# Performance work log

Measured on AMD Instinct MI355X. Metric: run time of the kernel, lower is better.

Reference implementation:

```python
import jax, jax.numpy as jnp
import numpy as np

WIN = 7  # skimage structural_similarity default win_size


def _uniform_valid(x):
    # x: [N, H, W] -> [N, H-6, W-6]; 7x7 uniform (box) filter, VALID.
    # exactly equivalent to uniform_filter + crop (boundary mode irrelevant).
    k = jnp.ones((1, 1, WIN, WIN), x.dtype) / (WIN * WIN)
    y = jax.lax.conv_general_dilated(x[:, None], k, (1, 1), 'VALID')
    return y[:, 0]


def _ssim_frames(x, y):
    # K1=0.01, K2=0.03, data_range=255, sample covariance (N/(N-1)).
    C1 = (0.01 * 255.0) ** 2
    C2 = (0.03 * 255.0) ** 2
    NP = WIN * WIN
    cov_norm = NP / (NP - 1.0)
    ux = _uniform_valid(x)
    uy = _uniform_valid(y)
    uxx = _uniform_valid(x * x)
    uyy = _uniform_valid(y * y)
    uxy = _uniform_valid(x * y)
    vx = cov_norm * (uxx - ux * ux)
    vy = cov_norm * (uyy - uy * uy)
    vxy = cov_norm * (uxy - ux * uy)
    S = ((2.0 * ux * uy + C1) * (2.0 * vxy + C2)) / (
        (ux * ux + uy * uy + C1) * (vx + vy + C2))
    return jnp.mean(S, axis=(1, 2))  # per-frame mean SSIM


def setup_inputs() -> dict:
    key = jax.random.key(0)
    k1, k2, k3 = jax.random.split(key, 3)
    B, T, C, H, W = 8, 20, 1, 512, 512
    gen_img = jax.random.uniform(k1, (B, T, C, H, W), dtype=jnp.float32)
    target = jax.random.uniform(k2, (B, T, C, H, W), dtype=jnp.float32)
    gen_D = jax.random.normal(k3, (B, 1), dtype=jnp.float32)
    return {"gen_img": gen_img, "target": target, "gen_D": gen_D}


def reference(gen_img, target, gen_D):
    B, T, C, H, W = gen_img.shape
    diff = gen_img - target
    L_rec = jnp.mean(jnp.abs(diff)) + jnp.mean(diff * diff)
    # SSIM on channel 0 of every frame, scaled by 255 (as in the numpy loop);
    # original detaches, so stop_gradient for faithfulness.
    x = gen_img[:, :, 0].reshape(B * T, H, W) * 255.0
    y = target[:, :, 0].reshape(B * T, H, W) * 255.0
    L_ssim = jnp.mean(jax.lax.stop_gradient(_ssim_frames(x, y)))
    L_adv = -jnp.mean(gen_D)
    L_total = L_rec + 0.01 * (1.0 - L_ssim) + 0.0001 * L_adv
    return (L_total, L_rec, L_ssim, L_adv)
```

## Files before the change

### kernel.cpp

```cpp
#include <hip/hip_runtime.h>

#define FRAMES 160
#define HH 512
#define WW 512
#define STRIPS 8
#define SROWS 64
#define NTOT 41943040
#define NBLK (STRIPS * FRAMES)


__device__ __forceinline__ float ssim_val(float Sx, float Sy, float Sxx,
                                          float Syy, float Sxy) {
  const float inv_np = 1.0f / 49.0f;
  const float cov = 49.0f / 48.0f;
  const float C1 = 1.0e-4f;
  const float C2 = 9.0e-4f;
  float ux = Sx * inv_np, uy = Sy * inv_np;
  float vx = cov * (Sxx * inv_np - ux * ux);
  float vy = cov * (Syy * inv_np - uy * uy);
  float vxy = cov * (Sxy * inv_np - ux * uy);
  float A1 = 2.0f * ux * uy + C1;
  float A2 = 2.0f * vxy + C2;
  float B1 = ux * ux + uy * uy + C1;
  float B2 = vx + vy + C2;
  return (A1 * A2) / (B1 * B2);
}

__global__ __launch_bounds__(256) void fused_kernel(
    const float* __restrict__ g, const float* __restrict__ t,
    float* __restrict__ ws) {
  const int strip = blockIdx.x;
  const int frame = blockIdx.y;
  const int row0 = strip * SROWS;
  const int rows = (strip == STRIPS - 1) ? 58 : 64;
  const int tid = threadIdx.x;
  const float* __restrict__ gf = g + (size_t)frame * (HH * WW) + tid * 2;
  const float* __restrict__ tf = t + (size_t)frame * (HH * WW) + tid * 2;

  __shared__ float2 buf[2][5][256];

  float2 xr[6], yr[6];
  float2 Sx = {0.f, 0.f}, Sy = {0.f, 0.f};
  float2 Sxx = {0.f, 0.f}, Syy = {0.f, 0.f}, Sxy = {0.f, 0.f};
  float sabs = 0.f, ssq = 0.f, ssum = 0.f;

  #pragma unroll
  for (int i = 0; i < 6; ++i) {
    float2 xv = *(const float2*)(gf + (row0 + i) * WW);
    float2 yv = *(const float2*)(tf + (row0 + i) * WW);
    xr[i] = xv; yr[i] = yv;
    float dx = xv.x - yv.x, dy = xv.y - yv.y;
    sabs += fabsf(dx) + fabsf(dy);
    ssq += dx * dx + dy * dy;
    Sx.x += xv.x; Sx.y += xv.y;
    Sy.x += yv.x; Sy.y += yv.y;
    Sxx.x += xv.x * xv.x; Sxx.y += xv.y * xv.y;
    Syy.x += yv.x * yv.x; Syy.y += yv.y * yv.y;
    Sxy.x += xv.x * yv.x; Sxy.y += xv.y * yv.y;
  }

  for (int r = 0; r < rows; ++r) {
    float2 nx = *(const float2*)(gf + (row0 + r + 6) * WW);
    float2 ny = *(const float2*)(tf + (row0 + r + 6) * WW);
    if (r < 58) {
      float dx = nx.x - ny.x, dy = nx.y - ny.y;
      sabs += fabsf(dx) + fabsf(dy);
      ssq += dx * dx + dy * dy;
    }
    Sx.x += nx.x; Sx.y += nx.y;
    Sy.x += ny.x; Sy.y += ny.y;
    Sxx.x += nx.x * nx.x; Sxx.y += nx.y * nx.y;
    Syy.x += ny.x * ny.x; Syy.y += ny.y * ny.y;
    Sxy.x += nx.x * ny.x; Sxy.y += nx.y * ny.y;

    const int par = r & 1;
    float px = Sx.x + Sx.y, py = Sy.x + Sy.y;
    float pxx = Sxx.x + Sxx.y, pyy = Syy.x + Syy.y, pxy = Sxy.x + Sxy.y;
    buf[par][0][tid] = make_float2(Sx.x, px);
    buf[par][1][tid] = make_float2(Sy.x, py);
    buf[par][2][tid] = make_float2(Sxx.x, pxx);
    buf[par][3][tid] = make_float2(Syy.x, pyy);
    buf[par][4][tid] = make_float2(Sxy.x, pxy);
    __syncthreads();

    if (tid < 253) {
      const float2* bx = buf[par][0];
      const float2* by = buf[par][1];
      const float2* bxx = buf[par][2];
      const float2* byy = buf[par][3];
      const float2* bxy = buf[par][4];
      float p1, p2; float2 f3;
      p1 = bx[tid + 1].y; p2 = bx[tid + 2].y; f3 = bx[tid + 3];
      float wxe = px + p1 + p2 + f3.x;
      float wxo = Sx.y + p1 + p2 + f3.y;
      p1 = by[tid + 1].y; p2 = by[tid + 2].y; f3 = by[tid + 3];
      float wye = py + p1 + p2 + f3.x;
      float wyo = Sy.y + p1 + p2 + f3.y;
      p1 = bxx[tid + 1].y; p2 = bxx[tid + 2].y; f3 = bxx[tid + 3];
      float wxxe = pxx + p1 + p2 + f3.x;
      float wxxo = Sxx.y + p1 + p2 + f3.y;
      p1 = byy[tid + 1].y; p2 = byy[tid + 2].y; f3 = byy[tid + 3];
      float wyye = pyy + p1 + p2 + f3.x;
      float wyyo = Syy.y + p1 + p2 + f3.y;
      p1 = bxy[tid + 1].y; p2 = bxy[tid + 2].y; f3 = bxy[tid + 3];
      float wxye = pxy + p1 + p2 + f3.x;
      float wxyo = Sxy.y + p1 + p2 + f3.y;

      ssum += ssim_val(wxe, wye, wxxe, wyye, wxye);
      ssum += ssim_val(wxo, wyo, wxxo, wyyo, wxyo);
    }

    float2 ox = xr[0], oy = yr[0];
    Sx.x -= ox.x; Sx.y -= ox.y;
    Sy.x -= oy.x; Sy.y -= oy.y;
    Sxx.x -= ox.x * ox.x; Sxx.y -= ox.y * ox.y;
    Syy.x -= oy.x * oy.x; Syy.y -= oy.y * oy.y;
    Sxy.x -= ox.x * oy.x; Sxy.y -= ox.y * oy.y;
    #pragma unroll
    for (int i = 0; i < 5; ++i) { xr[i] = xr[i + 1]; yr[i] = yr[i + 1]; }
    xr[5] = nx; yr[5] = ny;
  }

  #pragma unroll
  for (int off = 32; off > 0; off >>= 1) {
    sabs += __shfl_down(sabs, off, 64);
    ssq += __shfl_down(ssq, off, 64);
    ssum += __shfl_down(ssum, off, 64);
  }
  __syncthreads();
  float* scr = (float*)buf;
  const int lane = tid & 63, wv = tid >> 6;
  if (lane == 0) { scr[wv] = sabs; scr[4 + wv] = ssq; scr[8 + wv] = ssum; }
  __syncthreads();
  if (tid == 0) {
    const int bid = blockIdx.y * STRIPS + blockIdx.x;
    ws[bid] = scr[0] + scr[1] + scr[2] + scr[3];
    ws[NBLK + bid] = scr[4] + scr[5] + scr[6] + scr[7];
    ws[2 * NBLK + bid] = scr[8] + scr[9] + scr[10] + scr[11];
  }
}

__global__ __launch_bounds__(256) void finalize_kernel(
    const float* __restrict__ ws, const float* __restrict__ genD,
    float* __restrict__ out) {
  const int tid = threadIdx.x;
  float a = 0.f, b = 0.f, c = 0.f;
  for (int i = tid; i < NBLK; i += 256) {
    a += ws[i];
    b += ws[NBLK + i];
    c += ws[2 * NBLK + i];
  }
  #pragma unroll
  for (int off = 32; off > 0; off >>= 1) {
    a += __shfl_down(a, off, 64);
    b += __shfl_down(b, off, 64);
    c += __shfl_down(c, off, 64);
  }
  __shared__ float la[4], lb[4], lc[4];
  const int lane = tid & 63, wv = tid >> 6;
  if (lane == 0) { la[wv] = a; lb[wv] = b; lc[wv] = c; }
  __syncthreads();
  if (tid == 0) {
    a = la[0] + la[1] + la[2] + la[3];
    b = lb[0] + lb[1] + lb[2] + lb[3];
    c = lc[0] + lc[1] + lc[2] + lc[3];
    const float invN = 1.0f / (float)NTOT;
    float L_rec = a * invN + b * invN;
    float L_ssim = c / (160.0f * 506.0f * 506.0f);
    float d = 0.f;
    #pragma unroll
    for (int i = 0; i < 8; ++i) d += genD[i];
    float L_adv = -d / 8.0f;
    float L_total = L_rec + 0.01f * (1.0f - L_ssim) + 0.0001f * L_adv;
    out[0] = L_total;
    out[1] = L_rec;
    out[2] = L_ssim;
    out[3] = L_adv;
  }
}

extern "C" void kernel_launch(void* const* d_in, const int* in_sizes, int n_in,
                              void* d_out, int out_size, void* d_ws,
                              size_t ws_size, hipStream_t stream) {
  const float* gen_img = (const float*)d_in[0];
  const float* target = (const float*)d_in[1];
  const float* gen_D = (const float*)d_in[2];
  float* out = (float*)d_out;
  float* ws = (float*)d_ws;

  dim3 grid(STRIPS, FRAMES);
  fused_kernel<<<grid, 256, 0, stream>>>(gen_img, target, ws);
  finalize_kernel<<<1, 256, 0, stream>>>(ws, gen_D, out);
}
```

Before: 367.6 us.

## Restructure SSIM sliding window to float4 columns with two row groups per block

Result: slower. 375.9 us (+2.2%).

```diff
diff --git a/kernel.cpp b/kernel.cpp
--- a/kernel.cpp
+++ b/kernel.cpp
@@ -3,122 +3,124 @@
 #define FRAMES 160
 #define HH 512
 #define WW 512
-#define STRIPS 8
-#define SROWS 64
+#define STRIPS 16
+#define NBLK (STRIPS * FRAMES)
 #define NTOT 41943040
-#define NBLK (STRIPS * FRAMES)
 
-
-__device__ __forceinline__ float ssim_val(float Sx, float Sy, float Sxx,
-                                          float Syy, float Sxy) {
-  const float inv_np = 1.0f / 49.0f;
-  const float cov = 49.0f / 48.0f;
-  const float C1 = 1.0e-4f;
-  const float C2 = 9.0e-4f;
-  float ux = Sx * inv_np, uy = Sy * inv_np;
-  float vx = cov * (Sxx * inv_np - ux * ux);
-  float vy = cov * (Syy * inv_np - uy * uy);
-  float vxy = cov * (Sxy * inv_np - ux * uy);
-  float A1 = 2.0f * ux * uy + C1;
-  float A2 = 2.0f * vxy + C2;
-  float B1 = ux * ux + uy * uy + C1;
-  float B2 = vx + vy + C2;
-  return (A1 * A2) / (B1 * B2);
+__device__ __forceinline__ float ssim_fast(float a, float b, float sxx,
+                                           float syy, float sxy) {
+  const float K1 = 0.2401f;
+  const float K2 = 2.1609f;
+  const float cA = 49.0f / 24.0f;
+  const float cB = 49.0f / 48.0f;
+  float ab = a * b;
+  float s2 = fmaf(a, a, b * b);
+  float A1 = fmaf(2.0f, ab, K1);
+  float B1 = s2 + K1;
+  float A2 = fmaf(cA, fmaf(49.0f, sxy, -ab), K2);
+  float B2 = fmaf(cB, fmaf(49.0f, sxx + syy, -s2), K2);
+  return (A1 * A2) * __builtin_amdgcn_rcpf(B1 * B2);
 }
 
+#define HSTORE(S, P, A)                          \
+  P.x = S.x; P.y = P.x + S.y;                    \
+  P.z = P.y + S.z; P.w = P.z + S.w;              \
+  lds[grp][A][0][q] = make_float2(P.x, P.y);     \
+  lds[grp][A][1][q] = make_float2(P.z, P.w);
+
+#define HWIN(P, W, A) {                          \
+  float2 h1 = lds[grp][A][1][q + 1];             \
+  float2 l2 = lds[grp][A][0][q + 2];             \
+  W.x = P.w + h1.x;                              \
+  W.y = (P.w - P.x) + h1.y;                      \
+  W.z = (P.w - P.y) + (h1.y + l2.x);             \
+  W.w = (P.w - P.z) + (h1.y + l2.y); }
+
+#define LREC(xv, yv) {                                         \
+  float4 d_ = make_float4(xv.x - yv.x, xv.y - yv.y,            \
+                          xv.z - yv.z, xv.w - yv.w);           \
+  sabs += fabsf(d_.x) + fabsf(d_.y) + fabsf(d_.z) + fabsf(d_.w); \
+  ssq += d_.x * d_.x + d_.y * d_.y;                            \
+  ssq += d_.z * d_.z + d_.w * d_.w; }
+
+#define VADD(xv, yv)                                    \
+  Sx += xv; Sy += yv;                                   \
+  Sxx += xv * xv; Syy += yv * yv; Sxy += xv * yv;
+
+#define VSUB(xv, yv)                                    \
+  Sx -= xv; Sy -= yv;                                   \
+  Sxx -= xv * xv; Syy -= yv * yv; Sxy -= xv * yv;
+
 __global__ __launch_bounds__(256) void fused_kernel(
-    const float* __restrict__ g, const float* __restrict__ t,
+    const float* __restrict__ gsrc, const float* __restrict__ tsrc,
     float* __restrict__ ws) {
   const int strip = blockIdx.x;
   const int frame = blockIdx.y;
-  const int row0 = strip * SROWS;
-  const int rows = (strip == STRIPS - 1) ? 58 : 64;
+  const int row0 = strip * 32;
+  const int n_iter = (strip == STRIPS - 1) ? 13 : 16;
   const int tid = threadIdx.x;
-  const float* __restrict__ gf = g + (size_t)frame * (HH * WW) + tid * 2;
-  const float* __restrict__ tf = t + (size_t)frame * (HH * WW) + tid * 2;
+  const int grp = tid >> 7;
+  const int q = tid & 127;
 
-  __shared__ float2 buf[2][5][256];
+  const float* gp = gsrc + ((size_t)frame * HH + row0 + grp) * WW + q * 4;
+  const float* tp = tsrc + ((size_t)frame * HH + row0 + grp) * WW + q * 4;
 
-  float2 xr[6], yr[6];
-  float2 Sx = {0.f, 0.f}, Sy = {0.f, 0.f};
-  float2 Sxx = {0.f, 0.f}, Syy = {0.f, 0.f}, Sxy = {0.f, 0.f};
+  __shared__ float2 lds[2][5][2][132];
+
+  float4 Sx = make_float4(0.f, 0.f, 0.f, 0.f);
+  float4 Sy = Sx, Sxx = Sx, Syy = Sx, Sxy = Sx;
   float sabs = 0.f, ssq = 0.f, ssum = 0.f;
 
-  #pragma unroll
-  for (int i = 0; i < 6; ++i) {
-    float2 xv = *(const float2*)(gf + (row0 + i) * WW);
-    float2 yv = *(const float2*)(tf + (row0 + i) * WW);
-    xr[i] = xv; yr[i] = yv;
-    float dx = xv.x - yv.x, dy = xv.y - yv.y;
-    sabs += fabsf(dx) + fabsf(dy);
-    ssq += dx * dx + dy * dy;
-    Sx.x += xv.x; Sx.y += xv.y;
-    Sy.x += yv.x; Sy.y += yv.y;
-    Sxx.x += xv.x * xv.x; Sxx.y += xv.y * xv.y;
-    Syy.x += yv.x * yv.x; Syy.y += yv.y * yv.y;
-    Sxy.x += xv.x * yv.x; Sxy.y += xv.y * yv.y;
+  for (int i = 0; i < 7; ++i) {
+    float4 xv = *(const float4*)(gp + i * WW);
+    float4 yv = *(const float4*)(tp + i * WW);
+    VADD(xv, yv)
+    if (grp == 0) { LREC(xv, yv) }
   }
 
-  for (int r = 0; r < rows; ++r) {
-    float2 nx = *(const float2*)(gf + (row0 + r + 6) * WW);
-    float2 ny = *(const float2*)(tf + (row0 + r + 6) * WW);
-    if (r < 58) {
-      float dx = nx.x - ny.x, dy = nx.y - ny.y;
-      sabs += fabsf(dx) + fabsf(dy);
-      ssq += dx * dx + dy * dy;
-    }
-    Sx.x += nx.x; Sx.y += nx.y;
-    Sy.x += ny.x; Sy.y += ny.y;
-    Sxx.x += nx.x * nx.x; Sxx.y += nx.y * nx.y;
-    Syy.x += ny.x * ny.x; Syy.y += ny.y * ny.y;
-    Sxy.x += nx.x * ny.x; Sxy.y += nx.y * ny.y;
-
-    const int par = r & 1;
-    float px = Sx.x + Sx.y, py = Sy.x + Sy.y;
-    float pxx = Sxx.x + Sxx.y, pyy = Syy.x + Syy.y, pxy = Sxy.x + Sxy.y;
-    buf[par][0][tid] = make_float2(Sx.x, px);
-    buf[par][1][tid] = make_float2(Sy.x, py);
-    buf[par][2][tid] = make_float2(Sxx.x, pxx);
-    buf[par][3][tid] = make_float2(Syy.x, pyy);
-    buf[par][4][tid] = make_float2(Sxy.x, pxy);
+  for (int it = 0; it < n_iter; ++it) {
+    float4 Px, Py, Pxx, Pyy, Pxy;
+    HSTORE(Sx, Px, 0) HSTORE(Sy, Py, 1) HSTORE(Sxx, Pxx, 2)
+    HSTORE(Syy, Pyy, 3) HSTORE(Sxy, Pxy, 4)
+    __syncthreads();
+    float4 Wx, Wy, Wxx, Wyy, Wxy;
+    HWIN(Px, Wx, 0) HWIN(Py, Wy, 1) HWIN(Pxx, Wxx, 2)
+    HWIN(Pyy, Wyy, 3) HWIN(Pxy, Wxy, 4)
+    float v0 = ssim_fast(Wx.x, Wy.x, Wxx.x, Wyy.x, Wxy.x);
+    float v1 = ssim_fast(Wx.y, Wy.y, Wxx.y, Wyy.y, Wxy.y);
+    float v2 = ssim_fast(Wx.z, Wy.z, Wxx.z, Wyy.z, Wxy.z);
+    float v3 = ssim_fast(Wx.w, Wy.w, Wxx.w, Wyy.w, Wxy.w);
+    ssum += (q <= 126) ? v0 : 0.f;
+    ssum += (q <= 126) ? v1 : 0.f;
+    ssum += (q <= 125) ? v2 : 0.f;
+    ssum += (q <= 125) ? v3 : 0.f;
     __syncthreads();
 
-    if (tid < 253) {
-      const float2* bx = buf[par][0];
-      const float2* by = buf[par][1];
-      const float2* bxx = buf[par][2];
-      const float2* byy = buf[par][3];
-      const float2* bxy = buf[par][4];
-      float p1, p2; float2 f3;
-      p1 = bx[tid + 1].y; p2 = bx[tid + 2].y; f3 = bx[tid + 3];
-      float wxe = px + p1 + p2 + f3.x;
-      float wxo = Sx.y + p1 + p2 + f3.y;
-      p1 = by[tid + 1].y; p2 = by[tid + 2].y; f3 = by[tid + 3];
-      float wye = py + p1 + p2 + f3.x;
-      float wyo = Sy.y + p1 + p2 + f3.y;
-      p1 = bxx[tid + 1].y; p2 = bxx[tid + 2].y; f3 = bxx[tid + 3];
-      float wxxe = pxx + p1 + p2 + f3.x;
-      float wxxo = Sxx.y + p1 + p2 + f3.y;
-      p1 = byy[tid + 1].y; p2 = byy[tid + 2].y; f3 = byy[tid + 3];
-      float wyye = pyy + p1 + p2 + f3.x;
-      float wyyo = Syy.y + p1 + p2 + f3.y;
-      p1 = bxy[tid + 1].y; p2 = bxy[tid + 2].y; f3 = bxy[tid + 3];
-      float wxye = pxy + p1 + p2 + f3.x;
-      float wxyo = Sxy.y + p1 + p2 + f3.y;
-
-      ssum += ssim_val(wxe, wye, wxxe, wyye, wxye);
-      ssum += ssim_val(wxo, wyo, wxxo, wyyo, wxyo);
+    if (it + 1 < n_iter) {
+      const float* pn = gp + (size_t)(2 * it + 7) * WW;
+      const float* qn = tp + (size_t)(2 * it + 7) * WW;
+      const float* po = gp + (size_t)(2 * it) * WW;
+      const float* qo = tp + (size_t)(2 * it) * WW;
+      {
+        float4 nx = *(const float4*)pn;
+        float4 ny = *(const float4*)qn;
+        float4 ox = *(const float4*)po;
+        float4 oy = *(const float4*)qo;
+        VADD(nx, ny)
+        VSUB(ox, oy)
+        if ((grp == 0) && (2 * it + 7 <= 30)) { LREC(nx, ny) }
+      }
+      {
+        float4 nx = *(const float4*)(pn + WW);
+        float4 ny = *(const float4*)(qn + WW);
+        float4 ox = *(const float4*)(po + WW);
+        float4 oy = *(const float4*)(qo + WW);
+        VADD(nx, ny)
+        VSUB(ox, oy)
+        bool cnt = (grp == 0) ? (2 * it + 8 <= 30) : (2 * it + 9 == 31);
+        if (cnt) { LREC(nx, ny) }
+      }
     }
-
-    float2 ox = xr[0], oy = yr[0];
-    Sx.x -= ox.x; Sx.y -= ox.y;
-    Sy.x -= oy.x; Sy.y -= oy.y;
-    Sxx.x -= ox.x * ox.x; Sxx.y -= ox.y * ox.y;
-    Syy.x -= oy.x * oy.x; Syy.y -= oy.y * oy.y;
-    Sxy.x -= ox.x * oy.x; Sxy.y -= ox.y * oy.y;
-    #pragma unroll
-    for (int i = 0; i < 5; ++i) { xr[i] = xr[i + 1]; yr[i] = yr[i + 1]; }
-    xr[5] = nx; yr[5] = ny;
   }
 
   #pragma unroll
@@ -127,8 +129,7 @@
     ssq += __shfl_down(ssq, off, 64);
     ssum += __shfl_down(ssum, off, 64);
   }
-  __syncthreads();
-  float* scr = (float*)buf;
+  float* scr = (float*)&lds[0][0][0][0];
   const int lane = tid & 63, wv = tid >> 6;
   if (lane == 0) { scr[wv] = sabs; scr[4 + wv] = ssq; scr[8 + wv] = ssum; }
   __syncthreads();
```
